# Kernel tuning notes

Hardware: AMD Instinct MI355X
Metric: run time of the kernel (lower is better)

## Reference

```python
import jax, jax.numpy as jnp
import numpy as np

L, N, C = 8192, 8, 3
DIM, DIM_OUT, K, RATIO = 64, 128, 16, 0.25
L2 = int(L * RATIO)  # 2048; note L % L2 == 0 (needed for the fmod quirk)
EPS = 1e-5


def layer_norm(x, g, b):
    m = jnp.mean(x, axis=-1, keepdims=True)
    v = jnp.mean(jnp.square(x - m), axis=-1, keepdims=True)  # biased var, as torch LayerNorm
    return (x - m) * jax.lax.rsqrt(v + EPS) * g + b


def mlp(x, w1, g1, b1, w2, g2, b2):
    h = x @ w1.T
    h = layer_norm(h, g1, b1)
    h = h @ w2.T
    h = layer_norm(h, g2, b2)
    return jax.nn.relu(h)


def setup_inputs() -> dict:
    key = jax.random.key(0)
    ks = jax.random.split(key, 5)
    coords = jax.random.normal(ks[0], (L, N, C), jnp.float32)
    features = jax.random.normal(ks[1], (L, N, DIM), jnp.float32)
    s1 = 1.0 / np.sqrt(DIM)
    s2 = 1.0 / np.sqrt(DIM_OUT)
    w1 = jax.random.uniform(ks[2], (DIM_OUT, DIM), jnp.float32, -s1, s1)
    w2 = jax.random.uniform(ks[3], (DIM_OUT, DIM_OUT), jnp.float32, -s2, s2)
    g1 = jnp.ones((DIM_OUT,), jnp.float32)
    b1 = jnp.zeros((DIM_OUT,), jnp.float32)
    g2 = jnp.ones((DIM_OUT,), jnp.float32)
    b2 = jnp.zeros((DIM_OUT,), jnp.float32)
    # RandomDecimate: random permutation of point indices, keep first L2 (same across batch)
    keep_idx = jax.random.permutation(ks[4], L)[:L2].astype(jnp.int32)
    return dict(coords=coords, features=features, w1=w1, g1=g1, b1=b1,
                w2=w2, g2=g2, b2=b2, keep_idx=keep_idx)


def reference(coords, features, w1, g1, b1, w2, g2, b2, keep_idx):
    # MLP on all points: [L, N, DIM_OUT]
    feats = mlp(features, w1, g1, b1, w2, g2, b2)
    # decimation: keep_coords [L2, N, C]
    keep_coords = coords[keep_idx]
    # per-batch KNN of kept points against all points
    c = coords.transpose(1, 0, 2)        # [N, L, C]
    kc = keep_coords.transpose(1, 0, 2)  # [N, L2, C]
    d2 = (jnp.sum(kc * kc, -1)[:, :, None]
          + jnp.sum(c * c, -1)[:, None, :]
          - 2.0 * jnp.einsum('nic,njc->nij', kc, c))  # [N, L2, L]
    _, nn_idx = jax.lax.top_k(-d2, K)    # [N, L2, K] indices into [0, L)
    # faithful to clusters.fmod_(L2) on flattened idx n*L+l (L % L2 == 0 => l % L2)
    nn_idx = nn_idx % L2
    # fused gather + amax pooling over K neighbors
    fT = feats.transpose(1, 0, 2)  # [N, L, DIM_OUT]
    gathered = jax.vmap(lambda f, idx: f[idx])(fT, nn_idx)  # [N, L2, K, DIM_OUT]
    pool_features = jnp.max(gathered, axis=2).transpose(1, 0, 2)  # [L2, N, DIM_OUT]
    return keep_coords, pool_features
```

## Files before the change

kernel.cpp:

```cpp
#include <hip/hip_runtime.h>
#include <stdint.h>

#define L_    8192
#define N_    8
#define L2_   2048
#define K_    16

typedef unsigned int uint;
typedef unsigned short ushort;
typedef unsigned long long u64;
typedef __attribute__((ext_vector_type(8))) short bh8;
typedef __attribute__((ext_vector_type(4))) float f32x4;

__device__ __forceinline__ ushort f2b(float f){
  uint u = __float_as_uint(f);
  return (ushort)((u + 0x7FFFu + ((u >> 16) & 1u)) >> 16);
}
__device__ __forceinline__ uint ford(float f){
  uint u = __float_as_uint(f);
  return u ^ ((uint)((int)u >> 31) | 0x80000000u);
}
__device__ __forceinline__ float unford(uint u){
  uint v = (u & 0x80000000u) ? (u ^ 0x80000000u) : ~u;
  return __uint_as_float(v);
}

__device__ __forceinline__ void ld8(float* t, const float* p){
  float4 a = *(const float4*)p; float4 b = *(const float4*)(p + 4);
  t[0]=a.x; t[1]=a.y; t[2]=a.z; t[3]=a.w; t[4]=b.x; t[5]=b.y; t[6]=b.z; t[7]=b.w;
}
__device__ __forceinline__ bh8 pack8(const float* v){
  bh8 r;
  #pragma unroll
  for (int j = 0; j < 8; ++j) r[j] = (short)f2b(v[j]);
  return r;
}

__global__ __launch_bounds__(256) void prep_pack_k(const float* __restrict__ coords,
                                                   const int* __restrict__ keep,
                                                   const float* __restrict__ w1,
                                                   const float* __restrict__ w2,
                                                   float4* __restrict__ cF,
                                                   float* __restrict__ out0,
                                                   ushort* __restrict__ pw1,
                                                   ushort* __restrict__ pw2){
  int blk = blockIdx.x;
  int tid = threadIdx.x;
  if (blk < 96){
    int e = blk * 256 + tid;
    if (e < 8192) pw1[e] = f2b(w1[e]);
    else          pw2[e - 8192] = f2b(w2[e - 8192]);
  } else if (blk < 352){
    int e = (blk - 96) * 256 + tid;
    int l = e >> 3, n = e & 7;
    const float* cr = coords + (size_t)e * 3;
    float x = cr[0], y = cr[1], z = cr[2];
    float cc;
    {
      #pragma clang fp contract(off)
      cc = x*x + y*y + z*z;
    }
    cF[n * L_ + l] = make_float4(x, y, z, cc);
  } else {
    int t = (blk - 352) * 256 + tid;
    int i = t / 24; int rem = t - i * 24;
    out0[t] = coords[(size_t)keep[i] * 24 + rem];
  }
}

__global__ __launch_bounds__(256) void mlp_k(const float* __restrict__ feat,
                                             const ushort* __restrict__ pw1,
                                             const float* __restrict__ g1,
                                             const float* __restrict__ b1,
                                             const ushort* __restrict__ pw2,
                                             const float* __restrict__ g2,
                                             const float* __restrict__ b2,
                                             uint* __restrict__ fBw){
  __shared__ ushort hlds[16 * 136];
  __shared__ float pm1[4][16], pv1[4][16], pm2[4][16], pv2[4][16];
  int tid = threadIdx.x;
  int lane = tid & 63;
  int h = __builtin_amdgcn_readfirstlane(tid >> 6);
  int quad = lane >> 4, c = lane & 15;
  int rowg = blockIdx.x * 16;

  bh8 a1[2];
  {
    int rg = rowg + c; int l = rg & 2047, nb = rg >> 11;
    const float* xr = feat + (size_t)((l << 3) + nb) * 64 + quad * 8;
    float t0[8];
    ld8(t0, xr);      a1[0] = pack8(t0);
    ld8(t0, xr + 32); a1[1] = pack8(t0);
  }

  f32x4 acc1[2];
  acc1[0] = (f32x4){0.f,0.f,0.f,0.f}; acc1[1] = (f32x4){0.f,0.f,0.f,0.f};
  #pragma unroll
  for (int s = 0; s < 2; ++s){
    #pragma unroll
    for (int t = 0; t < 2; ++t){
      bh8 wb = *(const bh8*)(pw1 + (size_t)(h * 32 + t * 16 + c) * 64 + s * 32 + quad * 8);
      acc1[t] = __builtin_amdgcn_mfma_f32_16x16x32_bf16(a1[s], wb, acc1[t], 0, 0, 0);
    }
  }

  #pragma unroll
  for (int r = 0; r < 4; ++r){
    float s = acc1[0][r] + acc1[1][r];
    #pragma unroll
    for (int m = 1; m < 16; m <<= 1) s += __shfl_xor(s, m, 16);
    if (c == 0) pm1[h][quad * 4 + r] = s;
  }
  __syncthreads();
  float mean1[4], rstd1[4];
  #pragma unroll
  for (int r = 0; r < 4; ++r){
    int row = quad * 4 + r;
    mean1[r] = (pm1[0][row] + pm1[1][row] + pm1[2][row] + pm1[3][row]) * 0.0078125f;
  }
  #pragma unroll
  for (int r = 0; r < 4; ++r){
    float d0 = acc1[0][r] - mean1[r], d1 = acc1[1][r] - mean1[r];
    float s = d0 * d0 + d1 * d1;
    #pragma unroll
    for (int m = 1; m < 16; m <<= 1) s += __shfl_xor(s, m, 16);
    if (c == 0) pv1[h][quad * 4 + r] = s;
  }
  __syncthreads();
  #pragma unroll
  for (int r = 0; r < 4; ++r){
    int row = quad * 4 + r;
    rstd1[r] = rsqrtf((pv1[0][row] + pv1[1][row] + pv1[2][row] + pv1[3][row]) * 0.0078125f + 1e-5f);
  }
  #pragma unroll
  for (int t = 0; t < 2; ++t){
    int col = h * 32 + t * 16 + c;
    float gv = g1[col], bv = b1[col];
    #pragma unroll
    for (int r = 0; r < 4; ++r){
      float v = (acc1[t][r] - mean1[r]) * rstd1[r] * gv + bv;
      hlds[(quad * 4 + r) * 136 + col] = f2b(v);
    }
  }
  __syncthreads();

  f32x4 acc2[2];
  acc2[0] = (f32x4){0.f,0.f,0.f,0.f}; acc2[1] = (f32x4){0.f,0.f,0.f,0.f};
  #pragma unroll
  for (int s = 0; s < 4; ++s){
    bh8 af = *(const bh8*)(hlds + c * 136 + s * 32 + quad * 8);
    #pragma unroll
    for (int t = 0; t < 2; ++t){
      bh8 wb = *(const bh8*)(pw2 + (size_t)(h * 32 + t * 16 + c) * 128 + s * 32 + quad * 8);
      acc2[t] = __builtin_amdgcn_mfma_f32_16x16x32_bf16(af, wb, acc2[t], 0, 0, 0);
    }
  }

  #pragma unroll
  for (int r = 0; r < 4; ++r){
    float s = acc2[0][r] + acc2[1][r];
    #pragma unroll
    for (int m = 1; m < 16; m <<= 1) s += __shfl_xor(s, m, 16);
    if (c == 0) pm2[h][quad * 4 + r] = s;
  }
  __syncthreads();
  float mean2[4], rstd2[4];
  #pragma unroll
  for (int r = 0; r < 4; ++r){
    int row = quad * 4 + r;
    mean2[r] = (pm2[0][row] + pm2[1][row] + pm2[2][row] + pm2[3][row]) * 0.0078125f;
  }
  #pragma unroll
  for (int r = 0; r < 4; ++r){
    float d0 = acc2[0][r] - mean2[r], d1 = acc2[1][r] - mean2[r];
    float s = d0 * d0 + d1 * d1;
    #pragma unroll
    for (int m = 1; m < 16; m <<= 1) s += __shfl_xor(s, m, 16);
    if (c == 0) pv2[h][quad * 4 + r] = s;
  }
  __syncthreads();
  #pragma unroll
  for (int r = 0; r < 4; ++r){
    int row = quad * 4 + r;
    rstd2[r] = rsqrtf((pv2[0][row] + pv2[1][row] + pv2[2][row] + pv2[3][row]) * 0.0078125f + 1e-5f);
  }
  #pragma unroll
  for (int t = 0; t < 2; ++t){
    int col = h * 32 + t * 16 + c;
    float gv = g2[col], bv = b2[col];
    #pragma unroll
    for (int r = 0; r < 4; ++r){
      float v = fmaxf((acc2[t][r] - mean2[r]) * rstd2[r] * gv + bv, 0.f);
      hlds[(quad * 4 + r) * 136 + col] = f2b(v);
    }
  }
  __syncthreads();

  {
    int row16 = tid >> 4, pos = (tid & 15) * 4;
    const uint* src = (const uint*)hlds + row16 * 68 + pos;
    uint* dst = fBw + (size_t)(rowg + row16) * 64 + pos;
    *(uint4*)dst = *(const uint4*)src;
  }
}

__device__ __forceinline__ u64 shfl64(u64 v, int src){
  int lo = __shfl((int)(uint)v, src, 64);
  int hi = __shfl((int)(uint)(v >> 32), src, 64);
  return ((u64)(uint)hi << 32) | (uint)lo;
}

__device__ __forceinline__ u64 bsort64(u64 key, int lane){
  #pragma unroll
  for (int k = 2; k <= 64; k <<= 1){
    #pragma unroll
    for (int j = k >> 1; j > 0; j >>= 1){
      u64 o = shfl64(key, lane ^ j);
      bool lower = (lane & j) == 0;
      bool down  = (lane & k) == 0;
      bool takeMin = (lower == down);
      bool oLess = o < key;
      key = (oLess == takeMin) ? o : key;
    }
  }
  return key;
}
__device__ __forceinline__ u64 bmerge64(u64 key, int lane){
  #pragma unroll
  for (int j = 32; j > 0; j >>= 1){
    u64 o = shfl64(key, lane ^ j);
    bool lower = (lane & j) == 0;
    bool oLess = o < key;
    key = (oLess == lower) ? o : key;
  }
  return key;
}

__device__ __attribute__((noinline)) u64 drainx(u64* ldsq, int qcount, int lane){
  u64 a = (lane < qcount) ? ldsq[lane] : ~0ull;
  a = bsort64(a, lane);
  if (qcount > 64){
    u64 b = (64 + lane < qcount) ? ldsq[64 + lane] : ~0ull;
    b = bsort64(b, lane);
    u64 br = shfl64(b, 63 - lane);
    a = a < br ? a : br;
    a = bmerge64(a, lane);
  }
  if (lane < 16) ldsq[lane] = a;
  return a;
}

__device__ __forceinline__ void updq(u64* ql, int& qc, int& nx, float& thr,
                                     float qw, int lane){
  int q = qc;
  u64 k0 = (lane < q) ? ql[lane] : ~0ull;
  u64 k1 = (64 + lane < q) ? ql[64 + lane] : ~0ull;
  uint h0 = (uint)(k0 >> 32), h1 = (uint)(k1 >> 32);
  uint m = h0 < h1 ? h0 : h1;
  uint v = 0u;
  #pragma unroll
  for (int b = 31; b >= 16; --b){
    uint tv = v | (1u << b);
    if (__popcll(__ballot(m < tv)) < 16) v = tv;
  }
  uint vb = (v >= 0xFFFF0000u) ? 0xFFFFFFFFu : (v + 0x10000u);

  bool kp0 = (h0 <= vb);
  u64 bal0 = __ballot(kp0);
  int r0 = __builtin_amdgcn_mbcnt_lo((uint)bal0, 0);
  r0 = __builtin_amdgcn_mbcnt_hi((uint)(bal0 >> 32), r0);
  if (kp0) ql[r0] = k0;
  int c0 = __popcll(bal0);
  bool kp1 = (h1 <= vb);
  u64 bal1 = __ballot(kp1);
  int r1 = __builtin_amdgcn_mbcnt_lo((uint)bal1, 0);
  r1 = __builtin_amdgcn_mbcnt_hi((uint)(bal1 >> 32), r1);
  if (kp1) ql[c0 + r1] = k1;
  int out = c0 + __popcll(bal1);

  uint hb = vb;
  if (out > 64){
    u64 a = drainx(ql, out, lane);
    hb = (uint)(shfl64(a, 15) >> 32);
    out = 16;
  }
  qc = out;
  nx = out + 33;
  thr = unford(hb) + 1e-3f - qw;
}

__global__ __launch_bounds__(256) void knn_pool_k(const float4* __restrict__ cF,
                                                  const int* __restrict__ keep,
                                                  const uint* __restrict__ fB32,
                                                  float* __restrict__ out1){
  __shared__ u64 q8[4][2][128];
  int tid = threadIdx.x, lane = tid & 63;
  int wv = tid >> 6;
  int g0 = blockIdx.x * 8 + wv * 2;
  int n = g0 >> 11;
  int i0 = g0 & 2047, i1 = i0 + 1;
  u64* qlA = q8[wv][0];
  u64* qlB = q8[wv][1];
  float4 qa = cF[(n << 13) + keep[i0]];
  float4 qb = cF[(n << 13) + keep[i1]];
  const float4* base = cF + (n << 13);

  float q2ax = -2.f * qa.x, q2ay = -2.f * qa.y, q2az = -2.f * qa.z;
  float q2bx = -2.f * qb.x, q2by = -2.f * qb.y, q2bz = -2.f * qb.z;
  float tA = 3.4e38f, tB = 3.4e38f;
  int qcA = 0, qcB = 0, nxA = 49, nxB = 49;

  #define PROC2(cf, jidx) { \
    float sA = __builtin_fmaf(q2ax,(cf).x, __builtin_fmaf(q2ay,(cf).y, __builtin_fmaf(q2az,(cf).z,(cf).w))); \
    float sB = __builtin_fmaf(q2bx,(cf).x, __builtin_fmaf(q2by,(cf).y, __builtin_fmaf(q2bz,(cf).z,(cf).w))); \
    u64 balA = __ballot(sA <= tA); \
    u64 balB = __ballot(sB <= tB); \
    if (balA){ \
      if (sA <= tA){ \
        float d2; \
        { \
          _Pragma("clang fp contract(off)") \
          float dot = qa.x*(cf).x + qa.y*(cf).y + qa.z*(cf).z; \
          d2 = (qa.w + (cf).w) - 2.0f * dot; \
        } \
        int rel = __builtin_amdgcn_mbcnt_lo((uint)balA, 0); \
        rel = __builtin_amdgcn_mbcnt_hi((uint)(balA >> 32), rel); \
        qlA[qcA + rel] = ((u64)ford(d2) << 32) | (uint)(jidx); \
      } \
      qcA += __popcll(balA); \
      if (qcA >= nxA) updq(qlA, qcA, nxA, tA, qa.w, lane); \
    } \
    if (balB){ \
      if (sB <= tB){ \
        float d2; \
        { \
          _Pragma("clang fp contract(off)") \
          float dot = qb.x*(cf).x + qb.y*(cf).y + qb.z*(cf).z; \
          d2 = (qb.w + (cf).w) - 2.0f * dot; \
        } \
        int rel = __builtin_amdgcn_mbcnt_lo((uint)balB, 0); \
        rel = __builtin_amdgcn_mbcnt_hi((uint)(balB >> 32), rel); \
        qlB[qcB + rel] = ((u64)ford(d2) << 32) | (uint)(jidx); \
      } \
      qcB += __popcll(balB); \
      if (qcB >= nxB) updq(qlB, qcB, nxB, tB, qb.w, lane); \
    } \
  }

  for (int b = 0; b < 128; b += 4){
    const float4* p = base + (b << 6) + lane;
    float4 c0 = p[0];
    float4 c1 = p[64];
    float4 c2 = p[128];
    float4 c3 = p[192];
    int j0 = (b << 6) + lane;
    PROC2(c0, j0);
    PROC2(c1, j0 + 64);
    PROC2(c2, j0 + 128);
    PROC2(c3, j0 + 192);
  }
  #undef PROC2

  u64 aA = drainx(qlA, qcA, lane);
  u64 aB = drainx(qlB, qcB, lane);

  const uint* frow = fB32 + ((size_t)(n << 11) << 6);
  float a0 = -3.4e38f, a1v = -3.4e38f, b0 = -3.4e38f, b1v = -3.4e38f;
  #pragma unroll
  for (int k = 0; k < 16; ++k){
    int idxA = (int)(shfl64(aA, k) & 2047u);
    int idxB = (int)(shfl64(aB, k) & 2047u);
    uint uA = frow[((size_t)idxA << 6) + lane];
    uint uB = frow[((size_t)idxB << 6) + lane];
    a0  = fmaxf(a0,  __uint_as_float((uA & 0xFFFFu) << 16));
    a1v = fmaxf(a1v, __uint_as_float((uA >> 16) << 16));
    b0  = fmaxf(b0,  __uint_as_float((uB & 0xFFFFu) << 16));
    b1v = fmaxf(b1v, __uint_as_float((uB >> 16) << 16));
  }
  float2* oA = (float2*)(out1 + (size_t)(i0 * 8 + n) * 128);
  float2* oB = (float2*)(out1 + (size_t)(i1 * 8 + n) * 128);
  oA[lane] = make_float2(a0, a1v);
  oB[lane] = make_float2(b0, b1v);
}

extern "C" void kernel_launch(void* const* d_in, const int* in_sizes, int n_in,
                              void* d_out, int out_size, void* d_ws, size_t ws_size,
                              hipStream_t stream){
  const float* coords = (const float*)d_in[0];
  const float* feat   = (const float*)d_in[1];
  const float* w1     = (const float*)d_in[2];
  const float* g1     = (const float*)d_in[3];
  const float* b1     = (const float*)d_in[4];
  const float* w2     = (const float*)d_in[5];
  const float* g2     = (const float*)d_in[6];
  const float* b2     = (const float*)d_in[7];
  const int*   keep   = (const int*)d_in[8];
  float* out0 = (float*)d_out;
  float* out1 = out0 + 49152;

  char* ws = (char*)d_ws;
  float4* cF  = (float4*)ws;
  ushort* fB  = (ushort*)(ws + (1 << 20));
  ushort* pw1 = (ushort*)(ws + (5 << 20));
  ushort* pw2 = pw1 + 8192;

  hipLaunchKernelGGL(prep_pack_k, dim3(544), dim3(256), 0, stream,
                     coords, keep, w1, w2, cF, out0, pw1, pw2);
  hipLaunchKernelGGL(mlp_k, dim3(1024), dim3(256), 0, stream,
                     feat, pw1, g1, b1, pw2, g2, b2, (uint*)fB);
  hipLaunchKernelGGL(knn_pool_k, dim3(2048), dim3(256), 0, stream,
                     cF, keep, (const uint*)fB, out1);
}
```

Before: 158.7 us.

## Fuse prep, MLP and KNN pooling into one persistent cooperative kernel

Merges the three kernels (weight/coord packing, bf16 MFMA MLP, KNN+max-pool) into a single cooperative persistent kernel that loops over virtual blocks and separates the phases with grid.sync(). The grid is sized from occupancy times CU count and capped at 1024, with the old three-launch path kept as a fallback if the cooperative launch fails. This aims to remove launch gaps and inter-kernel drain. It also lowers the queue drain threshold in updq from 64 to 31 candidates. The cost is grid-wide barriers, fewer blocks in the KNN phase than the original 2048 (each block loops), and register pressure from combining all phases in one kernel with launch bounds (256,2).

```diff
diff --git a/kernel.cpp b/kernel.cpp
--- a/kernel.cpp
+++ b/kernel.cpp
@@ -1,5 +1,8 @@
 #include <hip/hip_runtime.h>
+#include <hip/hip_cooperative_groups.h>
 #include <stdint.h>
+
+namespace cg = cooperative_groups;
 
 #define L_    8192
 #define N_    8
@@ -34,6 +37,357 @@
   #pragma unroll
   for (int j = 0; j < 8; ++j) r[j] = (short)f2b(v[j]);
   return r;
+}
+
+__device__ __forceinline__ u64 shfl64(u64 v, int src){
+  int lo = __shfl((int)(uint)v, src, 64);
+  int hi = __shfl((int)(uint)(v >> 32), src, 64);
+  return ((u64)(uint)hi << 32) | (uint)lo;
+}
+
+__device__ __forceinline__ u64 bsort64(u64 key, int lane){
+  #pragma unroll
+  for (int k = 2; k <= 64; k <<= 1){
+    #pragma unroll
+    for (int j = k >> 1; j > 0; j >>= 1){
+      u64 o = shfl64(key, lane ^ j);
+      bool lower = (lane & j) == 0;
+      bool down  = (lane & k) == 0;
+      bool takeMin = (lower == down);
+      bool oLess = o < key;
+      key = (oLess == takeMin) ? o : key;
+    }
+  }
+  return key;
+}
+__device__ __forceinline__ u64 bmerge64(u64 key, int lane){
+  #pragma unroll
+  for (int j = 32; j > 0; j >>= 1){
+    u64 o = shfl64(key, lane ^ j);
+    bool lower = (lane & j) == 0;
+    bool oLess = o < key;
+    key = (oLess == lower) ? o : key;
+  }
+  return key;
+}
+
+__device__ __attribute__((noinline)) u64 drainx(u64* ldsq, int qcount, int lane){
+  u64 a = (lane < qcount) ? ldsq[lane] : ~0ull;
+  a = bsort64(a, lane);
+  if (qcount > 64){
+    u64 b = (64 + lane < qcount) ? ldsq[64 + lane] : ~0ull;
+    b = bsort64(b, lane);
+    u64 br = shfl64(b, 63 - lane);
+    a = a < br ? a : br;
+    a = bmerge64(a, lane);
+  }
+  if (lane < 16) ldsq[lane] = a;
+  return a;
+}
+
+__device__ __forceinline__ void updq(u64* ql, int& qc, int& nx, float& thr,
+                                     float qw, int lane){
+  int q = qc;
+  u64 k0 = (lane < q) ? ql[lane] : ~0ull;
+  u64 k1 = (64 + lane < q) ? ql[64 + lane] : ~0ull;
+  uint h0 = (uint)(k0 >> 32), h1 = (uint)(k1 >> 32);
+  uint m = h0 < h1 ? h0 : h1;
+  uint v = 0u;
+  #pragma unroll
+  for (int b = 31; b >= 16; --b){
+    uint tv = v | (1u << b);
+    if (__popcll(__ballot(m < tv)) < 16) v = tv;
+  }
+  uint vb = (v >= 0xFFFF0000u) ? 0xFFFFFFFFu : (v + 0x10000u);
+
+  bool kp0 = (h0 <= vb);
+  u64 bal0 = __ballot(kp0);
+  int r0 = __builtin_amdgcn_mbcnt_lo((uint)bal0, 0);
+  r0 = __builtin_amdgcn_mbcnt_hi((uint)(bal0 >> 32), r0);
+  if (kp0) ql[r0] = k0;
+  int c0 = __popcll(bal0);
+  bool kp1 = (h1 <= vb);
+  u64 bal1 = __ballot(kp1);
+  int r1 = __builtin_amdgcn_mbcnt_lo((uint)bal1, 0);
+  r1 = __builtin_amdgcn_mbcnt_hi((uint)(bal1 >> 32), r1);
+  if (kp1) ql[c0 + r1] = k1;
+  int out = c0 + __popcll(bal1);
+
+  uint hb = vb;
+  if (out > 31){
+    u64 a = drainx(ql, out, lane);
+    hb = (uint)(shfl64(a, 15) >> 32);
+    out = 16;
+  }
+  qc = out;
+  nx = out + 33;
+  thr = unford(hb) + 1e-3f - qw;
+}
+
+__global__ __launch_bounds__(256, 2) void fused_k(const float* __restrict__ coords,
+                                                  const float* __restrict__ feat,
+                                                  const float* __restrict__ w1,
+                                                  const float* __restrict__ g1,
+                                                  const float* __restrict__ b1,
+                                                  const float* __restrict__ w2,
+                                                  const float* __restrict__ g2,
+                                                  const float* __restrict__ b2,
+                                                  const int* __restrict__ keep,
+                                                  float4* __restrict__ cF,
+                                                  float* __restrict__ out0,
+                                                  float* __restrict__ out1,
+                                                  uint* __restrict__ fB,
+                                                  ushort* __restrict__ pw1,
+                                                  ushort* __restrict__ pw2){
+  cg::grid_group grid = cg::this_grid();
+  __shared__ ushort hlds[16 * 136];
+  __shared__ float pm1[4][16], pv1[4][16], pm2[4][16], pv2[4][16];
+  __shared__ u64 q8[4][2][128];
+
+  int tid = threadIdx.x;
+  int lane = tid & 63;
+  int nb = gridDim.x;
+
+  for (int vb = blockIdx.x; vb < 544; vb += nb){
+    if (vb < 96){
+      int e = vb * 256 + tid;
+      if (e < 8192) pw1[e] = f2b(w1[e]);
+      else          pw2[e - 8192] = f2b(w2[e - 8192]);
+    } else if (vb < 352){
+      int e = (vb - 96) * 256 + tid;
+      int l = e >> 3, n = e & 7;
+      const float* cr = coords + (size_t)e * 3;
+      float x = cr[0], y = cr[1], z = cr[2];
+      float cc;
+      {
+        #pragma clang fp contract(off)
+        cc = x*x + y*y + z*z;
+      }
+      cF[n * L_ + l] = make_float4(x, y, z, cc);
+    } else {
+      int t = (vb - 352) * 256 + tid;
+      int i = t / 24; int rem = t - i * 24;
+      out0[t] = coords[(size_t)keep[i] * 24 + rem];
+    }
+  }
+  grid.sync();
+
+  {
+    int h = __builtin_amdgcn_readfirstlane(tid >> 6);
+    int quad = lane >> 4, c = lane & 15;
+    for (int vb = blockIdx.x; vb < 1024; vb += nb){
+      int rowg = vb * 16;
+
+      bh8 a1[2];
+      {
+        int rg = rowg + c; int l = rg & 2047, nbk = rg >> 11;
+        const float* xr = feat + (size_t)((l << 3) + nbk) * 64 + quad * 8;
+        float t0[8];
+        ld8(t0, xr);      a1[0] = pack8(t0);
+        ld8(t0, xr + 32); a1[1] = pack8(t0);
+      }
+
+      f32x4 acc1[2];
+      acc1[0] = (f32x4){0.f,0.f,0.f,0.f}; acc1[1] = (f32x4){0.f,0.f,0.f,0.f};
+      #pragma unroll
+      for (int s = 0; s < 2; ++s){
+        #pragma unroll
+        for (int t = 0; t < 2; ++t){
+          bh8 wb = *(const bh8*)(pw1 + (size_t)(h * 32 + t * 16 + c) * 64 + s * 32 + quad * 8);
+          acc1[t] = __builtin_amdgcn_mfma_f32_16x16x32_bf16(a1[s], wb, acc1[t], 0, 0, 0);
+        }
+      }
+
+      #pragma unroll
+      for (int r = 0; r < 4; ++r){
+        float s = acc1[0][r] + acc1[1][r];
+        #pragma unroll
+        for (int m = 1; m < 16; m <<= 1) s += __shfl_xor(s, m, 16);
+        if (c == 0) pm1[h][quad * 4 + r] = s;
+      }
+      __syncthreads();
+      float mean1[4], rstd1[4];
+      #pragma unroll
+      for (int r = 0; r < 4; ++r){
+        int row = quad * 4 + r;
+        mean1[r] = (pm1[0][row] + pm1[1][row] + pm1[2][row] + pm1[3][row]) * 0.0078125f;
+      }
+      #pragma unroll
+      for (int r = 0; r < 4; ++r){
+        float d0 = acc1[0][r] - mean1[r], d1 = acc1[1][r] - mean1[r];
+        float s = d0 * d0 + d1 * d1;
+        #pragma unroll
+        for (int m = 1; m < 16; m <<= 1) s += __shfl_xor(s, m, 16);
+        if (c == 0) pv1[h][quad * 4 + r] = s;
+      }
+      __syncthreads();
+      #pragma unroll
+      for (int r = 0; r < 4; ++r){
+        int row = quad * 4 + r;
+        rstd1[r] = rsqrtf((pv1[0][row] + pv1[1][row] + pv1[2][row] + pv1[3][row]) * 0.0078125f + 1e-5f);
+      }
+      #pragma unroll
+      for (int t = 0; t < 2; ++t){
+        int col = h * 32 + t * 16 + c;
+        float gv = g1[col], bv = b1[col];
+        #pragma unroll
+        for (int r = 0; r < 4; ++r){
+          float v = (acc1[t][r] - mean1[r]) * rstd1[r] * gv + bv;
+          hlds[(quad * 4 + r) * 136 + col] = f2b(v);
+        }
+      }
+      __syncthreads();
+
+      f32x4 acc2[2];
+      acc2[0] = (f32x4){0.f,0.f,0.f,0.f}; acc2[1] = (f32x4){0.f,0.f,0.f,0.f};
+      #pragma unroll
+      for (int s = 0; s < 4; ++s){
+        bh8 af = *(const bh8*)(hlds + c * 136 + s * 32 + quad * 8);
+        #pragma unroll
+        for (int t = 0; t < 2; ++t){
+          bh8 wb = *(const bh8*)(pw2 + (size_t)(h * 32 + t * 16 + c) * 128 + s * 32 + quad * 8);
+          acc2[t] = __builtin_amdgcn_mfma_f32_16x16x32_bf16(af, wb, acc2[t], 0, 0, 0);
+        }
+      }
+
+      #pragma unroll
+      for (int r = 0; r < 4; ++r){
+        float s = acc2[0][r] + acc2[1][r];
+        #pragma unroll
+        for (int m = 1; m < 16; m <<= 1) s += __shfl_xor(s, m, 16);
+        if (c == 0) pm2[h][quad * 4 + r] = s;
+      }
+      __syncthreads();
+      float mean2[4], rstd2[4];
+      #pragma unroll
+      for (int r = 0; r < 4; ++r){
+        int row = quad * 4 + r;
+        mean2[r] = (pm2[0][row] + pm2[1][row] + pm2[2][row] + pm2[3][row]) * 0.0078125f;
+      }
+      #pragma unroll
+      for (int r = 0; r < 4; ++r){
+        float d0 = acc2[0][r] - mean2[r], d1 = acc2[1][r] - mean2[r];
+        float s = d0 * d0 + d1 * d1;
+        #pragma unroll
+        for (int m = 1; m < 16; m <<= 1) s += __shfl_xor(s, m, 16);
+        if (c == 0) pv2[h][quad * 4 + r] = s;
+      }
+      __syncthreads();
+      #pragma unroll
+      for (int r = 0; r < 4; ++r){
+        int row = quad * 4 + r;
+        rstd2[r] = rsqrtf((pv2[0][row] + pv2[1][row] + pv2[2][row] + pv2[3][row]) * 0.0078125f + 1e-5f);
+      }
+      #pragma unroll
+      for (int t = 0; t < 2; ++t){
+        int col = h * 32 + t * 16 + c;
+        float gv = g2[col], bv = b2[col];
+        #pragma unroll
+        for (int r = 0; r < 4; ++r){
+          float v = fmaxf((acc2[t][r] - mean2[r]) * rstd2[r] * gv + bv, 0.f);
+          hlds[(quad * 4 + r) * 136 + col] = f2b(v);
+        }
+      }
+      __syncthreads();
+
+      {
+        int row16 = tid >> 4, pos = (tid & 15) * 4;
+        const uint* src = (const uint*)hlds + row16 * 68 + pos;
+        uint* dst = fB + (size_t)(rowg + row16) * 64 + pos;
+        *(uint4*)dst = *(const uint4*)src;
+      }
+    }
+  }
+  grid.sync();
+
+  int wv = tid >> 6;
+  u64* qlA = q8[wv][0];
+  u64* qlB = q8[wv][1];
+  for (int qg = blockIdx.x; qg < 2048; qg += nb){
+    int g0 = qg * 8 + wv * 2;
+    int n = g0 >> 11;
+    int i0 = g0 & 2047, i1 = i0 + 1;
+    const float4* base = cF + (n << 13);
+    float4 qa = base[keep[i0]];
+    float4 qb = base[keep[i1]];
+
+    float q2ax = -2.f * qa.x, q2ay = -2.f * qa.y, q2az = -2.f * qa.z;
+    float q2bx = -2.f * qb.x, q2by = -2.f * qb.y, q2bz = -2.f * qb.z;
+    float tA = 3.4e38f, tB = 3.4e38f;
+    int qcA = 0, qcB = 0, nxA = 49, nxB = 49;
+
+    #define PROC2(cf, jidx) { \
+      float sA = __builtin_fmaf(q2ax,(cf).x, __builtin_fmaf(q2ay,(cf).y, __builtin_fmaf(q2az,(cf).z,(cf).w))); \
+      float sB = __builtin_fmaf(q2bx,(cf).x, __builtin_fmaf(q2by,(cf).y, __builtin_fmaf(q2bz,(cf).z,(cf).w))); \
+      u64 balA = __ballot(sA <= tA); \
+      u64 balB = __ballot(sB <= tB); \
+      if (balA){ \
+        if (sA <= tA){ \
+          float d2; \
+          { \
+            _Pragma("clang fp contract(off)") \
+            float dot = qa.x*(cf).x + qa.y*(cf).y + qa.z*(cf).z; \
+            d2 = (qa.w + (cf).w) - 2.0f * dot; \
+          } \
+          int rel = __builtin_amdgcn_mbcnt_lo((uint)balA, 0); \
+          rel = __builtin_amdgcn_mbcnt_hi((uint)(balA >> 32), rel); \
+          qlA[qcA + rel] = ((u64)ford(d2) << 32) | (uint)(jidx); \
+        } \
+        qcA += __popcll(balA); \
+        if (qcA >= nxA) updq(qlA, qcA, nxA, tA, qa.w, lane); \
+      } \
+      if (balB){ \
+        if (sB <= tB){ \
+          float d2; \
+          { \
+            _Pragma("clang fp contract(off)") \
+            float dot = qb.x*(cf).x + qb.y*(cf).y + qb.z*(cf).z; \
+            d2 = (qb.w + (cf).w) - 2.0f * dot; \
+          } \
+          int rel = __builtin_amdgcn_mbcnt_lo((uint)balB, 0); \
+          rel = __builtin_amdgcn_mbcnt_hi((uint)(balB >> 32), rel); \
+          qlB[qcB + rel] = ((u64)ford(d2) << 32) | (uint)(jidx); \
+        } \
+        qcB += __popcll(balB); \
+        if (qcB >= nxB) updq(qlB, qcB, nxB, tB, qb.w, lane); \
+      } \
+    }
+
+    for (int b = 0; b < 128; b += 4){
+      const float4* p = base + (b << 6) + lane;
+      float4 c0 = p[0];
+      float4 c1 = p[64];
+      float4 c2 = p[128];
+      float4 c3 = p[192];
+      int j0 = (b << 6) + lane;
+      PROC2(c0, j0);
+      PROC2(c1, j0 + 64);
+      PROC2(c2, j0 + 128);
+      PROC2(c3, j0 + 192);
+    }
+    #undef PROC2
+
+    u64 aA = drainx(qlA, qcA, lane);
+    u64 aB = drainx(qlB, qcB, lane);
+
+    const uint* frow = fB + ((size_t)(n << 11) << 6);
+    float a0 = -3.4e38f, a1v = -3.4e38f, b0 = -3.4e38f, b1v = -3.4e38f;
+    #pragma unroll
+    for (int k = 0; k < 16; ++k){
+      int idxA = (int)(shfl64(aA, k) & 2047u);
+      int idxB = (int)(shfl64(aB, k) & 2047u);
+      uint uA = frow[((size_t)idxA << 6) + lane];
+      uint uB = frow[((size_t)idxB << 6) + lane];
+      a0  = fmaxf(a0,  __uint_as_float((uA & 0xFFFFu) << 16));
+      a1v = fmaxf(a1v, __uint_as_float((uA >> 16) << 16));
+      b0  = fmaxf(b0,  __uint_as_float((uB & 0xFFFFu) << 16));
+      b1v = fmaxf(b1v, __uint_as_float((uB >> 16) << 16));
+    }
+    float2* oA = (float2*)(out1 + (size_t)(i0 * 8 + n) * 128);
+    float2* oB = (float2*)(out1 + (size_t)(i1 * 8 + n) * 128);
+    oA[lane] = make_float2(a0, a1v);
+    oB[lane] = make_float2(b0, b1v);
+  }
 }
 
 __global__ __launch_bounds__(256) void prep_pack_k(const float* __restrict__ coords,
@@ -202,91 +556,6 @@
     uint* dst = fBw + (size_t)(rowg + row16) * 64 + pos;
     *(uint4*)dst = *(const uint4*)src;
   }
-}
-
-__device__ __forceinline__ u64 shfl64(u64 v, int src){
-  int lo = __shfl((int)(uint)v, src, 64);
-  int hi = __shfl((int)(uint)(v >> 32), src, 64);
-  return ((u64)(uint)hi << 32) | (uint)lo;
-}
-
-__device__ __forceinline__ u64 bsort64(u64 key, int lane){
-  #pragma unroll
-  for (int k = 2; k <= 64; k <<= 1){
-    #pragma unroll
-    for (int j = k >> 1; j > 0; j >>= 1){
-      u64 o = shfl64(key, lane ^ j);
-      bool lower = (lane & j) == 0;
-      bool down  = (lane & k) == 0;
-      bool takeMin = (lower == down);
-      bool oLess = o < key;
-      key = (oLess == takeMin) ? o : key;
-    }
-  }
-  return key;
-}
-__device__ __forceinline__ u64 bmerge64(u64 key, int lane){
-  #pragma unroll
-  for (int j = 32; j > 0; j >>= 1){
-    u64 o = shfl64(key, lane ^ j);
-    bool lower = (lane & j) == 0;
-    bool oLess = o < key;
-    key = (oLess == lower) ? o : key;
-  }
-  return key;
-}
-
-__device__ __attribute__((noinline)) u64 drainx(u64* ldsq, int qcount, int lane){
-  u64 a = (lane < qcount) ? ldsq[lane] : ~0ull;
-  a = bsort64(a, lane);
-  if (qcount > 64){
-    u64 b = (64 + lane < qcount) ? ldsq[64 + lane] : ~0ull;
-    b = bsort64(b, lane);
-    u64 br = shfl64(b, 63 - lane);
-    a = a < br ? a : br;
-    a = bmerge64(a, lane);
-  }
-  if (lane < 16) ldsq[lane] = a;
-  return a;
-}
-
-__device__ __forceinline__ void updq(u64* ql, int& qc, int& nx, float& thr,
-                                     float qw, int lane){
-  int q = qc;
-  u64 k0 = (lane < q) ? ql[lane] : ~0ull;
-  u64 k1 = (64 + lane < q) ? ql[64 + lane] : ~0ull;
-  uint h0 = (uint)(k0 >> 32), h1 = (uint)(k1 >> 32);
-  uint m = h0 < h1 ? h0 : h1;
-  uint v = 0u;
-  #pragma unroll
-  for (int b = 31; b >= 16; --b){
-    uint tv = v | (1u << b);
-    if (__popcll(__ballot(m < tv)) < 16) v = tv;
-  }
-  uint vb = (v >= 0xFFFF0000u) ? 0xFFFFFFFFu : (v + 0x10000u);
-
-  bool kp0 = (h0 <= vb);
-  u64 bal0 = __ballot(kp0);
-  int r0 = __builtin_amdgcn_mbcnt_lo((uint)bal0, 0);
-  r0 = __builtin_amdgcn_mbcnt_hi((uint)(bal0 >> 32), r0);
-  if (kp0) ql[r0] = k0;
-  int c0 = __popcll(bal0);
-  bool kp1 = (h1 <= vb);
-  u64 bal1 = __ballot(kp1);
-  int r1 = __builtin_amdgcn_mbcnt_lo((uint)bal1, 0);
-  r1 = __builtin_amdgcn_mbcnt_hi((uint)(bal1 >> 32), r1);
-  if (kp1) ql[c0 + r1] = k1;
-  int out = c0 + __popcll(bal1);
-
-  uint hb = vb;
-  if (out > 64){
-    u64 a = drainx(ql, out, lane);
-    hb = (uint)(shfl64(a, 15) >> 32);
-    out = 16;
-  }
-  qc = out;
-  nx = out + 33;
-  thr = unford(hb) + 1e-3f - qw;
 }
 
 __global__ __launch_bounds__(256) void knn_pool_k(const float4* __restrict__ cF,
@@ -400,14 +669,39 @@
 
   char* ws = (char*)d_ws;
   float4* cF  = (float4*)ws;
-  ushort* fB  = (ushort*)(ws + (1 << 20));
+  uint*   fB  = (uint*)(ws + (1 << 20));
   ushort* pw1 = (ushort*)(ws + (5 << 20));
   ushort* pw2 = pw1 + 8192;
 
-  hipLaunchKernelGGL(prep_pack_k, dim3(544), dim3(256), 0, stream,
-                     coords, keep, w1, w2, cF, out0, pw1, pw2);
-  hipLaunchKernelGGL(mlp_k, dim3(1024), dim3(256), 0, stream,
-                     feat, pw1, g1, b1, pw2, g2, b2, (uint*)fB);
-  hipLaunchKernelGGL(knn_pool_k, dim3(2048), dim3(256), 0, stream,
-                     cF, keep, (const uint*)fB, out1);
-}
+  static int coopGrid = 0;
+  if (coopGrid == 0){
+    int dev = 0;
+    hipGetDevice(&dev);
+    hipDeviceProp_t prop;
+    int cus = 256;
+    if (hipGetDeviceProperties(&prop, dev) == hipSuccess) cus = prop.multiProcessorCount;
+    int maxB = 0;
+    if (hipOccupancyMaxActiveBlocksPerMultiprocessor(&maxB, (const void*)fused_k, 256, 0)
+        != hipSuccess || maxB < 1)
+      maxB = 1;
+    long g = (long)maxB * cus;
+    if (g > 1024) g = 1024;
+    if (g < 1) g = 1;
+    coopGrid = (int)g;
+  }
+
+  void* args[] = {(void*)&coords, (void*)&feat, (void*)&w1, (void*)&g1,
+                  (void*)&b1, (void*)&w2, (void*)&g2, (void*)&b2,
+                  (void*)&keep, (void*)&cF, (void*)&out0, (void*)&out1,
+                  (void*)&fB, (void*)&pw1, (void*)&pw2};
+  hipError_t e = hipLaunchCooperativeKernel((const void*)fused_k, dim3(coopGrid),
+                                            dim3(256), args, 0, stream);
+  if (e != hipSuccess){
+    hipLaunchKernelGGL(prep_pack_k, dim3(544), dim3(256), 0, stream,
+                       coords, keep, w1, w2, cF, out0, pw1, pw2);
+    hipLaunchKernelGGL(mlp_k, dim3(1024), dim3(256), 0, stream,
+                       feat, pw1, g1, b1, pw2, g2, b2, fB);
+    hipLaunchKernelGGL(knn_pool_k, dim3(2048), dim3(256), 0, stream,
+                       cF, keep, fB, out1);
+  }
+}
```

Result: slower. 324.3 us (+104.3%).

## Spatially sort points into voxel order and prune KNN chunks by bounding boxes

Applied to the files above, without the earlier changes.

The prep kernel now counting-sorts each batch's points by a 16^3 voxel grid, storing the sorted coords, an original-index map, each point's position, and per-64-point chunk bounding boxes. The KNN kernel starts scanning at the query's own chunk and skips any chunk whose box lower bound exceeds the current k-th distance threshold, so most distance work and loads are meant to be avoided. The queue drain trigger is lowered so the threshold tightens earlier. Costs include an extra sort pass run by only 8 blocks, per-chunk shuffles and divergence, and the lost 4-way load unrolling. The fixed grid assumes coordinates roughly in [-4,4], but clamping keeps results correct.

```diff
diff --git a/kernel.cpp b/kernel.cpp
--- a/kernel.cpp
+++ b/kernel.cpp
@@ -40,31 +40,90 @@
                                                    const int* __restrict__ keep,
                                                    const float* __restrict__ w1,
                                                    const float* __restrict__ w2,
-                                                   float4* __restrict__ cF,
                                                    float* __restrict__ out0,
                                                    ushort* __restrict__ pw1,
-                                                   ushort* __restrict__ pw2){
+                                                   ushort* __restrict__ pw2,
+                                                   float4* __restrict__ sCF,
+                                                   uint* __restrict__ oIdx,
+                                                   uint* __restrict__ sPos,
+                                                   float4* __restrict__ cBB){
   int blk = blockIdx.x;
   int tid = threadIdx.x;
   if (blk < 96){
     int e = blk * 256 + tid;
     if (e < 8192) pw1[e] = f2b(w1[e]);
     else          pw2[e - 8192] = f2b(w2[e - 8192]);
-  } else if (blk < 352){
-    int e = (blk - 96) * 256 + tid;
-    int l = e >> 3, n = e & 7;
-    const float* cr = coords + (size_t)e * 3;
+    return;
+  }
+  if (blk < 288){
+    int t = (blk - 96) * 256 + tid;
+    int i = t / 24; int rem = t - i * 24;
+    out0[t] = coords[(size_t)keep[i] * 24 + rem];
+    return;
+  }
+  int n = blk - 288;
+  __shared__ uint hist[4096];
+  __shared__ uint wsum[4];
+  int lane = tid & 63, wv = tid >> 6;
+  for (int i = tid; i < 4096; i += 256) hist[i] = 0;
+  __syncthreads();
+  for (int t = tid; t < 8192; t += 256){
+    const float* cr = coords + ((size_t)t * 8 + n) * 3;
+    float x = cr[0], y = cr[1], z = cr[2];
+    int ix = (int)floorf((x + 4.f) * 2.f); ix = ix < 0 ? 0 : (ix > 15 ? 15 : ix);
+    int iy = (int)floorf((y + 4.f) * 2.f); iy = iy < 0 ? 0 : (iy > 15 ? 15 : iy);
+    int iz = (int)floorf((z + 4.f) * 2.f); iz = iz < 0 ? 0 : (iz > 15 ? 15 : iz);
+    atomicAdd(&hist[(ix << 8) | (iy << 4) | iz], 1u);
+  }
+  __syncthreads();
+  uint tt = 0;
+  #pragma unroll
+  for (int j = 0; j < 16; ++j) tt += hist[tid * 16 + j];
+  uint sc = tt;
+  #pragma unroll
+  for (int m = 1; m < 64; m <<= 1){
+    uint o = __shfl_up(sc, m, 64);
+    if (lane >= m) sc += o;
+  }
+  if (lane == 63) wsum[wv] = sc;
+  __syncthreads();
+  uint wbase = 0;
+  for (int w = 0; w < wv; ++w) wbase += wsum[w];
+  uint run = wbase + sc - tt;
+  #pragma unroll
+  for (int j = 0; j < 16; ++j){
+    uint v = hist[tid * 16 + j];
+    hist[tid * 16 + j] = run;
+    run += v;
+  }
+  __syncthreads();
+  for (int t = tid; t < 8192; t += 256){
+    const float* cr = coords + ((size_t)t * 8 + n) * 3;
     float x = cr[0], y = cr[1], z = cr[2];
     float cc;
     {
       #pragma clang fp contract(off)
       cc = x*x + y*y + z*z;
     }
-    cF[n * L_ + l] = make_float4(x, y, z, cc);
-  } else {
-    int t = (blk - 352) * 256 + tid;
-    int i = t / 24; int rem = t - i * 24;
-    out0[t] = coords[(size_t)keep[i] * 24 + rem];
+    int ix = (int)floorf((x + 4.f) * 2.f); ix = ix < 0 ? 0 : (ix > 15 ? 15 : ix);
+    int iy = (int)floorf((y + 4.f) * 2.f); iy = iy < 0 ? 0 : (iy > 15 ? 15 : iy);
+    int iz = (int)floorf((z + 4.f) * 2.f); iz = iz < 0 ? 0 : (iz > 15 ? 15 : iz);
+    uint pos = atomicAdd(&hist[(ix << 8) | (iy << 4) | iz], 1u);
+    sCF[(n << 13) + pos] = make_float4(x, y, z, cc);
+    oIdx[(n << 13) + pos] = (uint)t;
+    sPos[(n << 13) + t]   = pos;
+  }
+  __syncthreads();
+  if (tid < 128){
+    float4 mn = make_float4(3.4e38f, 3.4e38f, 3.4e38f, 0.f);
+    float4 mx = make_float4(-3.4e38f, -3.4e38f, -3.4e38f, 0.f);
+    for (int j = 0; j < 64; ++j){
+      float4 p = sCF[(n << 13) + tid * 64 + j];
+      mn.x = fminf(mn.x, p.x); mn.y = fminf(mn.y, p.y); mn.z = fminf(mn.z, p.z);
+      mx.x = fmaxf(mx.x, p.x); mx.y = fmaxf(mx.y, p.y); mx.z = fmaxf(mx.z, p.z);
+    }
+    cBB[(n << 8) + tid * 2]     = mn;
+    cBB[(n << 8) + tid * 2 + 1] = mx;
   }
 }
 
@@ -279,7 +338,7 @@
   int out = c0 + __popcll(bal1);
 
   uint hb = vb;
-  if (out > 64){
+  if (out > 31){
     u64 a = drainx(ql, out, lane);
     hb = (uint)(shfl64(a, 15) >> 32);
     out = 16;
@@ -289,7 +348,10 @@
   thr = unford(hb) + 1e-3f - qw;
 }
 
-__global__ __launch_bounds__(256) void knn_pool_k(const float4* __restrict__ cF,
+__global__ __launch_bounds__(256) void knn_pool_k(const float4* __restrict__ sCF,
+                                                  const uint* __restrict__ oIdx,
+                                                  const uint* __restrict__ sPos,
+                                                  const float4* __restrict__ cBB,
                                                   const int* __restrict__ keep,
                                                   const uint* __restrict__ fB32,
                                                   float* __restrict__ out1){
@@ -298,78 +360,77 @@
   int wv = tid >> 6;
   int g0 = blockIdx.x * 8 + wv * 2;
   int n = g0 >> 11;
-  int i0 = g0 & 2047, i1 = i0 + 1;
-  u64* qlA = q8[wv][0];
-  u64* qlB = q8[wv][1];
-  float4 qa = cF[(n << 13) + keep[i0]];
-  float4 qb = cF[(n << 13) + keep[i1]];
-  const float4* base = cF + (n << 13);
-
-  float q2ax = -2.f * qa.x, q2ay = -2.f * qa.y, q2az = -2.f * qa.z;
-  float q2bx = -2.f * qb.x, q2by = -2.f * qb.y, q2bz = -2.f * qb.z;
-  float tA = 3.4e38f, tB = 3.4e38f;
-  int qcA = 0, qcB = 0, nxA = 49, nxB = 49;
-
-  #define PROC2(cf, jidx) { \
-    float sA = __builtin_fmaf(q2ax,(cf).x, __builtin_fmaf(q2ay,(cf).y, __builtin_fmaf(q2az,(cf).z,(cf).w))); \
-    float sB = __builtin_fmaf(q2bx,(cf).x, __builtin_fmaf(q2by,(cf).y, __builtin_fmaf(q2bz,(cf).z,(cf).w))); \
-    u64 balA = __ballot(sA <= tA); \
-    u64 balB = __ballot(sB <= tB); \
-    if (balA){ \
-      if (sA <= tA){ \
-        float d2; \
-        { \
-          _Pragma("clang fp contract(off)") \
-          float dot = qa.x*(cf).x + qa.y*(cf).y + qa.z*(cf).z; \
-          d2 = (qa.w + (cf).w) - 2.0f * dot; \
-        } \
-        int rel = __builtin_amdgcn_mbcnt_lo((uint)balA, 0); \
-        rel = __builtin_amdgcn_mbcnt_hi((uint)(balA >> 32), rel); \
-        qlA[qcA + rel] = ((u64)ford(d2) << 32) | (uint)(jidx); \
-      } \
-      qcA += __popcll(balA); \
-      if (qcA >= nxA) updq(qlA, qcA, nxA, tA, qa.w, lane); \
-    } \
-    if (balB){ \
-      if (sB <= tB){ \
-        float d2; \
-        { \
-          _Pragma("clang fp contract(off)") \
-          float dot = qb.x*(cf).x + qb.y*(cf).y + qb.z*(cf).z; \
-          d2 = (qb.w + (cf).w) - 2.0f * dot; \
-        } \
-        int rel = __builtin_amdgcn_mbcnt_lo((uint)balB, 0); \
-        rel = __builtin_amdgcn_mbcnt_hi((uint)(balB >> 32), rel); \
-        qlB[qcB + rel] = ((u64)ford(d2) << 32) | (uint)(jidx); \
-      } \
-      qcB += __popcll(balB); \
-      if (qcB >= nxB) updq(qlB, qcB, nxB, tB, qb.w, lane); \
-    } \
-  }
-
-  for (int b = 0; b < 128; b += 4){
-    const float4* p = base + (b << 6) + lane;
-    float4 c0 = p[0];
-    float4 c1 = p[64];
-    float4 c2 = p[128];
-    float4 c3 = p[192];
-    int j0 = (b << 6) + lane;
-    PROC2(c0, j0);
-    PROC2(c1, j0 + 64);
-    PROC2(c2, j0 + 128);
-    PROC2(c3, j0 + 192);
-  }
-  #undef PROC2
-
-  u64 aA = drainx(qlA, qcA, lane);
-  u64 aB = drainx(qlB, qcB, lane);
+  int i0 = g0 & 2047;
+  const float4* base = sCF + (n << 13);
+  const uint* oix = oIdx + (n << 13);
+  const float4* bb = cBB + (n << 8);
+
+  u64 res[2];
+  #pragma unroll
+  for (int qi = 0; qi < 2; ++qi){
+    int iq = i0 + qi;
+    uint pos = sPos[(n << 13) + keep[iq]];
+    float4 qv = base[pos];
+    int cs = (int)(pos >> 6);
+    float qw = qv.w;
+    float q2x = -2.f * qv.x, q2y = -2.f * qv.y, q2z = -2.f * qv.z;
+
+    float lb0, lb1;
+    {
+      float4 mn = bb[lane * 2], mx = bb[lane * 2 + 1];
+      float dx = fmaxf(fmaxf(mn.x - qv.x, qv.x - mx.x), 0.f);
+      float dy = fmaxf(fmaxf(mn.y - qv.y, qv.y - mx.y), 0.f);
+      float dz = fmaxf(fmaxf(mn.z - qv.z, qv.z - mx.z), 0.f);
+      lb0 = __builtin_fmaf(dx, dx, __builtin_fmaf(dy, dy, dz * dz));
+      mn = bb[(lane + 64) * 2]; mx = bb[(lane + 64) * 2 + 1];
+      dx = fmaxf(fmaxf(mn.x - qv.x, qv.x - mx.x), 0.f);
+      dy = fmaxf(fmaxf(mn.y - qv.y, qv.y - mx.y), 0.f);
+      dz = fmaxf(fmaxf(mn.z - qv.z, qv.z - mx.z), 0.f);
+      lb1 = __builtin_fmaf(dx, dx, __builtin_fmaf(dy, dy, dz * dz));
+    }
+
+    float thr = 3.4e38f, d2thr = 3.4e38f;
+    int qc = 0, nx = 49;
+    u64* ql = q8[wv][qi];
+
+    for (int ii = 0; ii < 128; ++ii){
+      int c = (cs + ii) & 127;
+      float lbc = __shfl((c & 64) ? lb1 : lb0, c & 63, 64);
+      if (lbc > d2thr) continue;
+      int j = (c << 6) + lane;
+      float4 cf = base[j];
+      float s = __builtin_fmaf(q2x, cf.x, __builtin_fmaf(q2y, cf.y,
+                __builtin_fmaf(q2z, cf.z, cf.w)));
+      u64 bal = __ballot(s <= thr);
+      if (bal){
+        if (s <= thr){
+          float d2;
+          {
+            #pragma clang fp contract(off)
+            float dot = qv.x*cf.x + qv.y*cf.y + qv.z*cf.z;
+            d2 = (qw + cf.w) - 2.0f * dot;
+          }
+          uint oj = oix[j];
+          int rel = __builtin_amdgcn_mbcnt_lo((uint)bal, 0);
+          rel = __builtin_amdgcn_mbcnt_hi((uint)(bal >> 32), rel);
+          ql[qc + rel] = ((u64)ford(d2) << 32) | oj;
+        }
+        qc += __popcll(bal);
+        if (qc >= nx){
+          updq(ql, qc, nx, thr, qw, lane);
+          d2thr = thr + qw;
+        }
+      }
+    }
+    res[qi] = drainx(ql, qc, lane);
+  }
 
   const uint* frow = fB32 + ((size_t)(n << 11) << 6);
   float a0 = -3.4e38f, a1v = -3.4e38f, b0 = -3.4e38f, b1v = -3.4e38f;
   #pragma unroll
   for (int k = 0; k < 16; ++k){
-    int idxA = (int)(shfl64(aA, k) & 2047u);
-    int idxB = (int)(shfl64(aB, k) & 2047u);
+    int idxA = (int)(shfl64(res[0], k) & 2047u);
+    int idxB = (int)(shfl64(res[1], k) & 2047u);
     uint uA = frow[((size_t)idxA << 6) + lane];
     uint uB = frow[((size_t)idxB << 6) + lane];
     a0  = fmaxf(a0,  __uint_as_float((uA & 0xFFFFu) << 16));
@@ -378,7 +439,7 @@
     b1v = fmaxf(b1v, __uint_as_float((uB >> 16) << 16));
   }
   float2* oA = (float2*)(out1 + (size_t)(i0 * 8 + n) * 128);
-  float2* oB = (float2*)(out1 + (size_t)(i1 * 8 + n) * 128);
+  float2* oB = (float2*)(out1 + (size_t)((i0 + 1) * 8 + n) * 128);
   oA[lane] = make_float2(a0, a1v);
   oB[lane] = make_float2(b0, b1v);
 }
@@ -399,15 +460,18 @@
   float* out1 = out0 + 49152;
 
   char* ws = (char*)d_ws;
-  float4* cF  = (float4*)ws;
-  ushort* fB  = (ushort*)(ws + (1 << 20));
-  ushort* pw1 = (ushort*)(ws + (5 << 20));
-  ushort* pw2 = pw1 + 8192;
-
-  hipLaunchKernelGGL(prep_pack_k, dim3(544), dim3(256), 0, stream,
-                     coords, keep, w1, w2, cF, out0, pw1, pw2);
+  uint*   fB   = (uint*)ws;
+  ushort* pw1  = (ushort*)(ws + (4 << 20));
+  ushort* pw2  = pw1 + 8192;
+  float4* sCF  = (float4*)(ws + (4 << 20) + (64 << 10));
+  uint*   oIdx = (uint*)(ws + (5 << 20) + (64 << 10));
+  uint*   sPos = oIdx + 65536;
+  float4* cBB  = (float4*)(ws + (5 << 20) + (576 << 10));
+
+  hipLaunchKernelGGL(prep_pack_k, dim3(296), dim3(256), 0, stream,
+                     coords, keep, w1, w2, out0, pw1, pw2, sCF, oIdx, sPos, cBB);
   hipLaunchKernelGGL(mlp_k, dim3(1024), dim3(256), 0, stream,
-                     feat, pw1, g1, b1, pw2, g2, b2, (uint*)fB);
+                     feat, pw1, g1, b1, pw2, g2, b2, fB);
   hipLaunchKernelGGL(knn_pool_k, dim3(2048), dim3(256), 0, stream,
-                     cF, keep, (const uint*)fB, out1);
-}
+                     sCF, oIdx, sPos, cBB, keep, fB, out1);
+}
```

Result: slower. 185.0 us (+16.5%).
